# Optimization experiments

Measured on AMD Instinct MI355X. Metric: run time of the kernel, lower is better.

The kernel has to match this reference:

```python
import jax, jax.numpy as jnp
import numpy as np

ROPE_BASE = 10000.0


def _rope_cos_sin(seq_len, head_size, dtype):
    inv_freq = 1.0 / (ROPE_BASE ** (jnp.arange(0, head_size, 2, dtype=jnp.float32) / head_size))
    t = jnp.arange(seq_len, dtype=jnp.float32)
    freqs = jnp.outer(t, inv_freq)            # [S, D/2]
    emb = jnp.concatenate([freqs, freqs], axis=-1)  # [S, D]
    return jnp.cos(emb).astype(dtype), jnp.sin(emb).astype(dtype)


def _rotate_half(x):
    d = x.shape[-1] // 2
    return jnp.concatenate([-x[..., d:], x[..., :d]], axis=-1)


def setup_inputs() -> dict:
    key = jax.random.key(0)
    k1, k2, k3 = jax.random.split(key, 3)
    B, S, H, D = 2, 2048, 32, 128
    NUM_BLOCKS, BLOCK_SIZE = 512, 16
    q = jax.random.normal(k1, (B, S, H, D), dtype=jnp.float32)
    k = jax.random.normal(k2, (B, S, H, D), dtype=jnp.float32)
    v = jax.random.normal(k3, (B, S, H, D), dtype=jnp.float32)
    k_cache = jnp.zeros((NUM_BLOCKS, H, D, BLOCK_SIZE), dtype=jnp.float32)
    v_cache = jnp.zeros((NUM_BLOCKS, H, D, BLOCK_SIZE), dtype=jnp.float32)
    context_lengths = jnp.full((B,), S, dtype=jnp.int64)
    block_tables = jnp.arange(B * (S // BLOCK_SIZE), dtype=jnp.int64).reshape(B, S // BLOCK_SIZE)
    return {"q": q, "k": k, "v": v, "k_cache": k_cache, "v_cache": v_cache,
            "context_lengths": context_lengths, "block_tables": block_tables}


def reference(q, k, v, k_cache, v_cache, context_lengths, block_tables):
    # PagedAttention.pad_context_forward (prefill path, lengths == seq_len, block-aligned)
    B, S, H, D = q.shape
    block_size = k_cache.shape[-1]
    n_blk = S // block_size

    qt = q.transpose(0, 2, 1, 3)  # [B,H,S,D]
    kt = k.transpose(0, 2, 1, 3)
    vt = v.transpose(0, 2, 1, 3)

    cos, sin = _rope_cos_sin(S, D, q.dtype)  # [S,D], broadcast over B,H
    q_rot = qt * cos + _rotate_half(qt) * sin
    k_rot = kt * cos + _rotate_half(kt) * sin

    # copy_to_cache (prefill): scatter rotated keys and raw values into paged caches
    def to_blocks(x_bshd):  # [B,S,H,D] -> [B*n_blk, H, D, block_size]
        xb = x_bshd.reshape(B, n_blk, block_size, H, D)
        return xb.transpose(0, 1, 3, 4, 2).reshape(B * n_blk, H, D, block_size)

    k_cache_new = k_cache.at[block_tables.reshape(-1)].set(to_blocks(k_rot.transpose(0, 2, 1, 3)))
    v_cache_new = v_cache.at[block_tables.reshape(-1)].set(to_blocks(v))

    # dense causal attention, fp32 softmax
    scores = jnp.einsum('bhqd,bhkd->bhqk', q_rot, k_rot) / jnp.sqrt(jnp.asarray(D, q.dtype))
    causal = jnp.tril(jnp.ones((S, S), dtype=bool))
    scores = scores + jnp.where(causal, jnp.asarray(0.0, q.dtype), jnp.finfo(q.dtype).min)
    weights = jax.nn.softmax(scores.astype(jnp.float32), axis=-1).astype(q.dtype)
    out = jnp.einsum('bhqk,bhkd->bhqd', weights, vt)  # note: original uses un-rotated v
    attn_output = out.transpose(0, 2, 1, 3).reshape(B, S, H * D)
    return attn_output, k_cache_new, v_cache_new
```

## Files before the change

kernel.cpp:

```cpp
#include <hip/hip_runtime.h>
#include <math.h>

#define B 2
#define S 2048
#define H 32
#define D 128
#define BS 16
#define NBLK (S / BS)
#define NT 256

#define FREQ_C 0.20762050593045953f
#define SCALE 0.08838834764831845f

typedef __attribute__((ext_vector_type(8))) short short8;
typedef __attribute__((ext_vector_type(4))) float floatx4;

__device__ __forceinline__ unsigned short f2bf(float x) {
  return (unsigned short)((__float_as_uint(x) + 0x8000u) >> 16);
}
__device__ __forceinline__ unsigned packbf(float lo, float hi) {
  unsigned ua = __float_as_uint(lo) + 0x8000u;
  unsigned ub = __float_as_uint(hi) + 0x8000u;
  return (ub & 0xFFFF0000u) | (ua >> 16);
}

__device__ __forceinline__ void gload_lds16(const void* g, void* l) {
  __builtin_amdgcn_global_load_lds(
      (const __attribute__((address_space(1))) void*)g,
      (__attribute__((address_space(3))) void*)l, 16, 0, 0);
}

__global__ __launch_bounds__(256) void build_tbl(float* __restrict__ tbl) {
  int i = blockIdx.x * 256 + threadIdx.x;
  int s = i >> 6, j = i & 63;
  float fr = exp2f(-(float)j * FREQ_C);
  float sn, cs;
  sincosf((float)s * fr, &sn, &cs);
  tbl[s * 128 + j] = cs;
  tbl[s * 128 + 64 + j] = sn;
}

__global__ __launch_bounds__(512) void map_blocks(
    const int* __restrict__ bt, int* __restrict__ bitmap) {
  int t = threadIdx.x;
  bitmap[t] = 0;
  __syncthreads();
  if (t < B * NBLK) bitmap[bt[t]] = 1;
}

__global__ __launch_bounds__(256) void zero_unmapped(
    const int* __restrict__ bitmap, float* __restrict__ k_out,
    float* __restrict__ v_out) {
  int p = blockIdx.x;
  if (bitmap[p]) return;
  size_t base = (size_t)p * (H * D * BS) + (size_t)blockIdx.y * 8192;
  float4 z = {0.f, 0.f, 0.f, 0.f};
  float4* kd = (float4*)(k_out + base);
  float4* vd = (float4*)(v_out + base);
#pragma unroll
  for (int i = 0; i < 8; ++i) {
    kd[i * 256 + threadIdx.x] = z;
    vd[i * 256 + threadIdx.x] = z;
  }
}

__global__ __launch_bounds__(NT) void rope_scatter2(
    const float* __restrict__ k, const float* __restrict__ v,
    const int* __restrict__ block_tables,
    float* __restrict__ k_out, float* __restrict__ v_out,
    unsigned short* __restrict__ kvb, const float* __restrict__ tbl) {
  int idx = blockIdx.x;
  int h = idx % H;
  int m = idx / H;
  int b = m / NBLK;
  int sblk = m % NBLK;
  int phys = block_tables[m];

  __shared__ float Ks[BS][D + 4];
  __shared__ float Vs[BS][D + 4];
  __shared__ float Kr[BS][D + 4];
  __shared__ float Tc[BS][D + 4];
  int tid = threadIdx.x;

  const size_t in_base = (((size_t)b * S + (size_t)sblk * BS) * H + h) * D;
  const float* trow = tbl + (size_t)sblk * BS * 128;
  for (int p = 0; p < (BS * D) / NT; ++p) {
    int f = p * NT + tid;
    int row = f >> 7, d = f & 127;
    size_t g = in_base + (size_t)row * (H * D) + d;
    Ks[row][d] = k[g];
    Vs[row][d] = v[g];
    Tc[row][d] = trow[row * 128 + d];
  }
  __syncthreads();

  size_t out_base = ((size_t)phys * H + h) * (D * BS);
  for (int p = 0; p < (BS * D) / NT; ++p) {
    int f = p * NT + tid;
    int d = f >> 4, t = f & 15;
    float cs = Tc[t][d & 63];
    float sn = Tc[t][64 + (d & 63)];
    float x = Ks[t][d];
    float xr = (d < 64) ? -Ks[t][d + 64] : Ks[t][d - 64];
    float r = x * cs + xr * sn;
    k_out[out_base + f] = r;
    v_out[out_base + f] = Vs[t][d];
    Kr[t][d] = r;
  }
  __syncthreads();

  const int kt = sblk >> 2, cb = sblk & 3;
  const size_t tb = ((size_t)(b * H + h) * (S / 64) + kt) * 16384;
  unsigned* kb32 = (unsigned*)(kvb + tb) + (size_t)cb * 16 * 64;
  for (int p = 0; p < (BS * D / 2) / NT; ++p) {
    int e = p * NT + tid;
    int t = e >> 6, dp = e & 63;
    float2 kr2 = *(const float2*)&Kr[t][2 * dp];
    kb32[t * 64 + (dp ^ ((t & 7) << 2))] = packbf(kr2.x, kr2.y);
  }
  unsigned* vb32 = (unsigned*)(kvb + tb + 8192);
  for (int p = 0; p < (BS * D / 2) / NT; ++p) {
    int e = p * NT + tid;
    int d = e >> 3, tp = e & 7;
    vb32[d * 32 + ((cb * 8 + tp) ^ ((d & 7) << 2))] =
        packbf(Vs[2 * tp][d], Vs[2 * tp + 1][d]);
  }
}

__global__ __launch_bounds__(512, 4) void attn_mfma4(
    const float* __restrict__ q, const unsigned short* __restrict__ kvb,
    const float* __restrict__ tbl, float* __restrict__ out) {
  __shared__ unsigned short KV[2][16384];
  __shared__ unsigned short Pb[8][16][64];

  const int wgid = blockIdx.x;
  const int slot = wgid >> 3;
  const int bh = (slot >> 4) * 8 + (wgid & 7);
  const int qt = 15 - (slot & 15);
  const int b = bh >> 5, h = bh & 31;
  const int tid = threadIdx.x;
  const int lane = tid & 63, w = tid >> 6;
  const int n = lane & 15, quad = lane >> 4;

  short8 qf[4];
  {
    const int sq = qt * 128 + w * 16 + n;
    const float* qr = q + (((size_t)b * S + sq) * H + h) * D;
    const float* tr = tbl + (size_t)sq * 128;
#pragma unroll
    for (int ks = 0; ks < 4; ++ks) {
      int d0 = ks * 32 + quad * 8;
      float x[8], p[8], cs[8], sn[8];
      *(float4*)&x[0] = *(const float4*)(qr + d0);
      *(float4*)&x[4] = *(const float4*)(qr + d0 + 4);
      *(float4*)&p[0] = *(const float4*)(qr + (d0 ^ 64));
      *(float4*)&p[4] = *(const float4*)(qr + (d0 ^ 64) + 4);
      int dm = d0 & 63;
      *(float4*)&cs[0] = *(const float4*)(tr + dm);
      *(float4*)&cs[4] = *(const float4*)(tr + dm + 4);
      *(float4*)&sn[0] = *(const float4*)(tr + 64 + dm);
      *(float4*)&sn[4] = *(const float4*)(tr + 64 + dm + 4);
      unsigned short tmp[8];
#pragma unroll
      for (int i = 0; i < 8; ++i) {
        float r = (d0 < 64) ? (x[i] * cs[i] - p[i] * sn[i])
                            : (x[i] * cs[i] + p[i] * sn[i]);
        tmp[i] = f2bf(r * SCALE);
      }
      qf[ks] = *(short8*)tmp;
    }
  }

  const floatx4 zero = {0.f, 0.f, 0.f, 0.f};
  floatx4 Ot[8];
#pragma unroll
  for (int dt = 0; dt < 8; ++dt) Ot[dt] = zero;
  float m_run[4], l_run[4];
#pragma unroll
  for (int r = 0; r < 4; ++r) {
    m_run[r] = -INFINITY;
    l_run[r] = 0.f;
  }

  const unsigned short* KVg = kvb + (size_t)bh * (S / 64) * 16384;

  auto STAGE = [&](int buf, int t2) {
    const char* src =
        (const char*)(KVg + (size_t)t2 * 16384) + w * 4096 + (lane << 4);
    char* dst = (char*)&KV[buf][0] + w * 4096;
#pragma unroll
    for (int i = 0; i < 4; ++i) gload_lds16(src + i * 1024, dst + i * 1024);
  };

  const int last = 2 * qt + 1;
  int cur = 0;
  STAGE(0, 0);
  __syncthreads();

  const int sw = (n & 7) << 4;

  for (int kt = 0; kt <= last; ++kt) {
    if (kt < last) STAGE(cur ^ 1, kt + 1);

    const bool active = (kt * 64 <= qt * 128 + w * 16 + 15);
    if (active) {
      const char* Kb = (const char*)&KV[cur][0];
      const char* Vb = Kb + 16384;

      floatx4 acc[4];
#pragma unroll
      for (int ct = 0; ct < 4; ++ct) {
        floatx4 a = zero;
#pragma unroll
        for (int ks = 0; ks < 4; ++ks) {
          short8 kf = *(const short8*)(
              Kb + (((ct * 16 + n) * 256 + ks * 64 + quad * 16) ^ sw));
          a = __builtin_amdgcn_mfma_f32_16x16x32_bf16(qf[ks], kf, a, 0, 0, 0);
        }
        acc[ct] = a;
      }

      if (kt >= 2 * qt) {
        int lim = w * 16 + quad * 4 - (kt - 2 * qt) * 64;
#pragma unroll
        for (int ct = 0; ct < 4; ++ct)
#pragma unroll
          for (int r = 0; r < 4; ++r)
            if (ct * 16 + n > lim + r) acc[ct][r] = -INFINITY;
      }

      float mnew[4], alpha[4], rs[4];
#pragma unroll
      for (int r = 0; r < 4; ++r) {
        float v =
            fmaxf(fmaxf(acc[0][r], acc[1][r]), fmaxf(acc[2][r], acc[3][r]));
        v = fmaxf(v, __shfl_xor(v, 1));
        v = fmaxf(v, __shfl_xor(v, 2));
        v = fmaxf(v, __shfl_xor(v, 4));
        v = fmaxf(v, __shfl_xor(v, 8));
        mnew[r] = fmaxf(m_run[r], v);
        alpha[r] = __expf(m_run[r] - mnew[r]);
        m_run[r] = mnew[r];
      }
      float pv[4][4];
#pragma unroll
      for (int r = 0; r < 4; ++r) rs[r] = 0.f;
#pragma unroll
      for (int ct = 0; ct < 4; ++ct)
#pragma unroll
        for (int r = 0; r < 4; ++r) {
          float e = __expf(acc[ct][r] - mnew[r]);
          pv[ct][r] = e;
          rs[r] += e;
        }
#pragma unroll
      for (int r = 0; r < 4; ++r) {
        float s = rs[r];
        s += __shfl_xor(s, 1);
        s += __shfl_xor(s, 2);
        s += __shfl_xor(s, 4);
        s += __shfl_xor(s, 8);
        l_run[r] = l_run[r] * alpha[r] + s;
      }

#pragma unroll
      for (int dt = 0; dt < 8; ++dt)
#pragma unroll
        for (int r = 0; r < 4; ++r) Ot[dt][r] *= alpha[r];

#pragma unroll
      for (int ct = 0; ct < 4; ++ct)
#pragma unroll
        for (int r = 0; r < 4; ++r) {
          int row = quad * 4 + r;
          Pb[w][row][(ct * 16 + n) ^ ((row & 7) << 3)] = f2bf(pv[ct][r]);
        }
      __builtin_amdgcn_wave_barrier();

      short8 pf0 = *(const short8*)&Pb[w][n][(quad * 8) ^ ((n & 7) << 3)];
      short8 pf1 = *(const short8*)&Pb[w][n][(32 + quad * 8) ^ ((n & 7) << 3)];
#pragma unroll
      for (int dt = 0; dt < 8; ++dt) {
        short8 vf0 = *(const short8*)(
            Vb + (((dt * 16 + n) * 128 + quad * 16) ^ sw));
        short8 vf1 = *(const short8*)(
            Vb + (((dt * 16 + n) * 128 + 64 + quad * 16) ^ sw));
        Ot[dt] =
            __builtin_amdgcn_mfma_f32_16x16x32_bf16(pf0, vf0, Ot[dt], 0, 0, 0);
        Ot[dt] =
            __builtin_amdgcn_mfma_f32_16x16x32_bf16(pf1, vf1, Ot[dt], 0, 0, 0);
      }
    }
    __syncthreads();
    cur ^= 1;
  }

  float linv[4];
#pragma unroll
  for (int r = 0; r < 4; ++r) linv[r] = 1.f / l_run[r];
#pragma unroll
  for (int r = 0; r < 4; ++r) {
    int row = qt * 128 + w * 16 + quad * 4 + r;
    float* orow = out + ((size_t)(b * S + row) * H + h) * D + n;
#pragma unroll
    for (int dt = 0; dt < 8; ++dt) orow[dt * 16] = Ot[dt][r] * linv[r];
  }
}

__global__ __launch_bounds__(NT) void rope_scatter(
    const float* __restrict__ k, const float* __restrict__ v,
    const int* __restrict__ block_tables,
    float* __restrict__ k_out, float* __restrict__ v_out) {
  int idx = blockIdx.x;
  int h = idx % H;
  int m = idx / H;
  int b = m / NBLK;
  int sblk = m % NBLK;
  int phys = block_tables[m];

  __shared__ float Ks[BS][D + 4];
  __shared__ float Vs[BS][D + 4];
  int tid = threadIdx.x;

  const size_t in_base = (((size_t)b * S + (size_t)sblk * BS) * H + h) * D;
  for (int p = 0; p < (BS * D) / NT; ++p) {
    int f = p * NT + tid;
    int row = f >> 7, d = f & 127;
    size_t g = in_base + (size_t)row * (H * D) + d;
    Ks[row][d] = k[g];
    Vs[row][d] = v[g];
  }
  __syncthreads();

  size_t out_base = ((size_t)phys * H + h) * (D * BS);
  for (int p = 0; p < (BS * D) / NT; ++p) {
    int f = p * NT + tid;
    int d = f >> 4, t = f & 15;
    int s = sblk * BS + t;
    float fr = exp2f(-(float)(d & 63) * FREQ_C);
    float sn, cs;
    sincosf((float)s * fr, &sn, &cs);
    float x = Ks[t][d];
    float xr = (d < 64) ? -Ks[t][d + 64] : Ks[t][d - 64];
    k_out[out_base + f] = x * cs + xr * sn;
    v_out[out_base + f] = Vs[t][d];
  }
}

__global__ __launch_bounds__(NT, 3) void attn_mfma(
    const float* __restrict__ q, const float* __restrict__ kc,
    const float* __restrict__ vc, const int* __restrict__ bt,
    float* __restrict__ out) {
  __shared__ unsigned short Ks[64][136];
  __shared__ unsigned short Vt[128][72];
  __shared__ unsigned short Pb[4][16][72];

  const int qt = (S / 64 - 1) - (int)blockIdx.x;
  const int bh = blockIdx.y;
  const int b = bh >> 5, h = bh & 31;
  const int tid = threadIdx.x;
  const int lane = tid & 63, w = tid >> 6;
  const int n = lane & 15, quad = lane >> 4;

  short8 qf[4];
  {
    const int sq = qt * 64 + w * 16 + n;
    const float* qr = q + (((size_t)b * S + sq) * H + h) * D;
#pragma unroll
    for (int ks = 0; ks < 4; ++ks) {
      int d0 = ks * 32 + quad * 8;
      float x[8], p[8];
      *(float4*)&x[0] = *(const float4*)(qr + d0);
      *(float4*)&x[4] = *(const float4*)(qr + d0 + 4);
      *(float4*)&p[0] = *(const float4*)(qr + (d0 ^ 64));
      *(float4*)&p[4] = *(const float4*)(qr + (d0 ^ 64) + 4);
      unsigned short tmp[8];
#pragma unroll
      for (int i = 0; i < 8; ++i) {
        int d = d0 + i;
        float fr = exp2f(-(float)(d & 63) * FREQ_C);
        float sn, cs;
        __sincosf((float)sq * fr, &sn, &cs);
        float r = (d < 64) ? (x[i] * cs - p[i] * sn) : (x[i] * cs + p[i] * sn);
        tmp[i] = f2bf(r * SCALE);
      }
      qf[ks] = *(short8*)tmp;
    }
  }

  const floatx4 zero = {0.f, 0.f, 0.f, 0.f};
  floatx4 Ot[8];
#pragma unroll
  for (int dt = 0; dt < 8; ++dt) Ot[dt] = zero;
  float m_run[4], l_run[4];
#pragma unroll
  for (int r = 0; r < 4; ++r) {
    m_run[r] = -INFINITY;
    l_run[r] = 0.f;
  }

  for (int kt = 0; kt <= qt; ++kt) {
    int m4 = b * NBLK + kt * 4;
#pragma unroll
    for (int cb = 0; cb < 4; ++cb) {
      const size_t cbase = ((size_t)bt[m4 + cb] * H + h) * (D * BS);
      const float* ks_src = kc + cbase;
      const float* vs_src = vc + cbase;
#pragma unroll
      for (int it = 0; it < 4; ++it) {
        int rem = it * NT + tid;
        int dp = rem >> 4, t = rem & 15;
        float a0 = ks_src[(2 * dp) * BS + t];
        float a1 = ks_src[(2 * dp + 1) * BS + t];
        *(unsigned*)&Ks[cb * 16 + t][2 * dp] = packbf(a0, a1);
      }
#pragma unroll
      for (int it = 0; it < 4; ++it) {
        int rem = it * NT + tid;
        int d = rem >> 3, tp = rem & 7;
        float2 vv = *(const float2*)(vs_src + d * BS + tp * 2);
        *(unsigned*)&Vt[d][cb * 16 + tp * 2] = packbf(vv.x, vv.y);
      }
    }
    __syncthreads();

    floatx4 acc[4];
#pragma unroll
    for (int ct = 0; ct < 4; ++ct) {
      floatx4 a = zero;
#pragma unroll
      for (int ks = 0; ks < 4; ++ks) {
        short8 kf = *(const short8*)&Ks[ct * 16 + n][ks * 32 + quad * 8];
        a = __builtin_amdgcn_mfma_f32_16x16x32_bf16(qf[ks], kf, a, 0, 0, 0);
      }
      acc[ct] = a;
    }

    if (kt == qt) {
#pragma unroll
      for (int ct = 0; ct < 4; ++ct)
#pragma unroll
        for (int r = 0; r < 4; ++r)
          if (ct * 16 + n > w * 16 + quad * 4 + r) acc[ct][r] = -INFINITY;
    }

    float mnew[4], alpha[4], rs[4];
#pragma unroll
    for (int r = 0; r < 4; ++r) {
      float v = fmaxf(fmaxf(acc[0][r], acc[1][r]), fmaxf(acc[2][r], acc[3][r]));
      v = fmaxf(v, __shfl_xor(v, 1));
      v = fmaxf(v, __shfl_xor(v, 2));
      v = fmaxf(v, __shfl_xor(v, 4));
      v = fmaxf(v, __shfl_xor(v, 8));
      mnew[r] = fmaxf(m_run[r], v);
      alpha[r] = __expf(m_run[r] - mnew[r]);
      m_run[r] = mnew[r];
    }
    float pv[4][4];
#pragma unroll
    for (int r = 0; r < 4; ++r) rs[r] = 0.f;
#pragma unroll
    for (int ct = 0; ct < 4; ++ct)
#pragma unroll
      for (int r = 0; r < 4; ++r) {
        float e = __expf(acc[ct][r] - mnew[r]);
        pv[ct][r] = e;
        rs[r] += e;
      }
#pragma unroll
    for (int r = 0; r < 4; ++r) {
      float s = rs[r];
      s += __shfl_xor(s, 1);
      s += __shfl_xor(s, 2);
      s += __shfl_xor(s, 4);
      s += __shfl_xor(s, 8);
      l_run[r] = l_run[r] * alpha[r] + s;
    }

#pragma unroll
    for (int dt = 0; dt < 8; ++dt)
#pragma unroll
      for (int r = 0; r < 4; ++r) Ot[dt][r] *= alpha[r];

#pragma unroll
    for (int ct = 0; ct < 4; ++ct)
#pragma unroll
      for (int r = 0; r < 4; ++r)
        Pb[w][quad * 4 + r][ct * 16 + n] = f2bf(pv[ct][r]);
    __builtin_amdgcn_wave_barrier();

    short8 pf0 = *(const short8*)&Pb[w][n][quad * 8];
    short8 pf1 = *(const short8*)&Pb[w][n][32 + quad * 8];
#pragma unroll
    for (int dt = 0; dt < 8; ++dt) {
      short8 vf0 = *(const short8*)&Vt[dt * 16 + n][quad * 8];
      short8 vf1 = *(const short8*)&Vt[dt * 16 + n][32 + quad * 8];
      Ot[dt] = __builtin_amdgcn_mfma_f32_16x16x32_bf16(pf0, vf0, Ot[dt], 0, 0, 0);
      Ot[dt] = __builtin_amdgcn_mfma_f32_16x16x32_bf16(pf1, vf1, Ot[dt], 0, 0, 0);
    }
    __syncthreads();
  }

  float linv[4];
#pragma unroll
  for (int r = 0; r < 4; ++r) linv[r] = 1.f / l_run[r];
#pragma unroll
  for (int r = 0; r < 4; ++r) {
    int row = qt * 64 + w * 16 + quad * 4 + r;
    float* orow = out + ((size_t)(b * S + row) * H + h) * D + n;
#pragma unroll
    for (int dt = 0; dt < 8; ++dt) orow[dt * 16] = Ot[dt][r] * linv[r];
  }
}

extern "C" void kernel_launch(void* const* d_in, const int* in_sizes, int n_in,
                              void* d_out, int out_size, void* d_ws,
                              size_t ws_size, hipStream_t stream) {
  const float* q = (const float*)d_in[0];
  const float* k = (const float*)d_in[1];
  const float* v = (const float*)d_in[2];
  const int* block_tables = (const int*)d_in[6];

  float* out_attn = (float*)d_out;
  float* out_kc = out_attn + (size_t)B * S * H * D;
  float* out_vc = out_kc + (size_t)512 * H * D * BS;

  const size_t kvb_shorts = (size_t)B * H * (S / 64) * 16384;
  const size_t tbl_floats = (size_t)S * 128;
  const size_t need = kvb_shorts * 2 + tbl_floats * 4 + 2048;

  if (d_ws != nullptr && ws_size >= need) {
    unsigned short* kvb = (unsigned short*)d_ws;
    float* tbl = (float*)(kvb + kvb_shorts);
    int* bitmap = (int*)(tbl + tbl_floats);

    map_blocks<<<1, 512, 0, stream>>>(block_tables, bitmap);
    zero_unmapped<<<dim3(512, 8), 256, 0, stream>>>(bitmap, out_kc, out_vc);

    build_tbl<<<(S * 64) / 256, 256, 0, stream>>>(tbl);
    rope_scatter2<<<B * NBLK * H, NT, 0, stream>>>(k, v, block_tables, out_kc,
                                                   out_vc, kvb, tbl);
    attn_mfma4<<<(S / 128) * B * H, 512, 0, stream>>>(q, kvb, tbl, out_attn);
  } else {
    hipMemsetAsync(out_kc, 0, (size_t)512 * H * D * BS * sizeof(float), stream);
    hipMemsetAsync(out_vc, 0, (size_t)512 * H * D * BS * sizeof(float), stream);
    rope_scatter<<<B * NBLK * H, NT, 0, stream>>>(k, v, block_tables, out_kc,
                                                  out_vc);
    dim3 grid(S / 64, B * H);
    attn_mfma<<<grid, NT, 0, stream>>>(q, out_kc, out_vc, block_tables,
                                       out_attn);
  }
}
```

Before: 854.3 us.

## Use lazy softmax rescaling, deferred row-sum reduction and MFMA priority hints

Flash-attention online softmax now rescales the running max and output accumulators only when some row's new max exceeds the stored max by more than a threshold of 8, checked with a wave vote. Per-lane partial row sums are kept and reduced across lanes once at the end instead of every tile. s_setprio is raised around the QK and PV MFMA loops to favour matrix issue. This removes per-tile shuffles and accumulator rescaling, but allows stale maxima, so exp values can reach up to e^8 before normalisation.

```diff
diff --git a/kernel.cpp b/kernel.cpp
--- a/kernel.cpp
+++ b/kernel.cpp
@@ -127,7 +127,7 @@
   }
 }
 
-__global__ __launch_bounds__(512, 4) void attn_mfma4(
+__global__ __launch_bounds__(512, 4) void attn_mfma5(
     const float* __restrict__ q, const unsigned short* __restrict__ kvb,
     const float* __restrict__ tbl, float* __restrict__ out) {
   __shared__ unsigned short KV[2][16384];
@@ -175,11 +175,11 @@
   floatx4 Ot[8];
 #pragma unroll
   for (int dt = 0; dt < 8; ++dt) Ot[dt] = zero;
-  float m_run[4], l_run[4];
+  float m_run[4], l_part[4];
 #pragma unroll
   for (int r = 0; r < 4; ++r) {
     m_run[r] = -INFINITY;
-    l_run[r] = 0.f;
+    l_part[r] = 0.f;
   }
 
   const unsigned short* KVg = kvb + (size_t)bh * (S / 64) * 16384;
@@ -208,6 +208,7 @@
       const char* Vb = Kb + 16384;
 
       floatx4 acc[4];
+      __builtin_amdgcn_s_setprio(1);
 #pragma unroll
       for (int ct = 0; ct < 4; ++ct) {
         floatx4 a = zero;
@@ -219,6 +220,7 @@
         }
         acc[ct] = a;
       }
+      __builtin_amdgcn_s_setprio(0);
 
       if (kt >= 2 * qt) {
         int lim = w * 16 + quad * 4 - (kt - 2 * qt) * 64;
@@ -229,44 +231,38 @@
             if (ct * 16 + n > lim + r) acc[ct][r] = -INFINITY;
       }
 
-      float mnew[4], alpha[4], rs[4];
-#pragma unroll
-      for (int r = 0; r < 4; ++r) {
-        float v =
+      float rmax[4];
+#pragma unroll
+      for (int r = 0; r < 4; ++r)
+        rmax[r] =
             fmaxf(fmaxf(acc[0][r], acc[1][r]), fmaxf(acc[2][r], acc[3][r]));
-        v = fmaxf(v, __shfl_xor(v, 1));
-        v = fmaxf(v, __shfl_xor(v, 2));
-        v = fmaxf(v, __shfl_xor(v, 4));
-        v = fmaxf(v, __shfl_xor(v, 8));
-        mnew[r] = fmaxf(m_run[r], v);
-        alpha[r] = __expf(m_run[r] - mnew[r]);
-        m_run[r] = mnew[r];
+      bool ok = true;
+#pragma unroll
+      for (int r = 0; r < 4; ++r) ok = ok && (rmax[r] - m_run[r] <= 8.f);
+      if (!__all(ok ? 1 : 0)) {
+#pragma unroll
+        for (int r = 0; r < 4; ++r) {
+          float v = rmax[r];
+          v = fmaxf(v, __shfl_xor(v, 1));
+          v = fmaxf(v, __shfl_xor(v, 2));
+          v = fmaxf(v, __shfl_xor(v, 4));
+          v = fmaxf(v, __shfl_xor(v, 8));
+          float mnew = fmaxf(m_run[r], v);
+          float alpha = __expf(m_run[r] - mnew);
+          m_run[r] = mnew;
+          l_part[r] *= alpha;
+#pragma unroll
+          for (int dt = 0; dt < 8; ++dt) Ot[dt][r] *= alpha;
+        }
       }
       float pv[4][4];
 #pragma unroll
-      for (int r = 0; r < 4; ++r) rs[r] = 0.f;
-#pragma unroll
       for (int ct = 0; ct < 4; ++ct)
 #pragma unroll
-        for (int r = 0; r < 4; ++r) {
-          float e = __expf(acc[ct][r] - mnew[r]);
-          pv[ct][r] = e;
-          rs[r] += e;
-        }
-#pragma unroll
-      for (int r = 0; r < 4; ++r) {
-        float s = rs[r];
-        s += __shfl_xor(s, 1);
-        s += __shfl_xor(s, 2);
-        s += __shfl_xor(s, 4);
-        s += __shfl_xor(s, 8);
-        l_run[r] = l_run[r] * alpha[r] + s;
-      }
-
-#pragma unroll
-      for (int dt = 0; dt < 8; ++dt)
-#pragma unroll
-        for (int r = 0; r < 4; ++r) Ot[dt][r] *= alpha[r];
+        for (int r = 0; r < 4; ++r) pv[ct][r] = __expf(acc[ct][r] - m_run[r]);
+#pragma unroll
+      for (int r = 0; r < 4; ++r)
+        l_part[r] += (pv[0][r] + pv[1][r]) + (pv[2][r] + pv[3][r]);
 
 #pragma unroll
       for (int ct = 0; ct < 4; ++ct)
@@ -279,6 +275,7 @@
 
       short8 pf0 = *(const short8*)&Pb[w][n][(quad * 8) ^ ((n & 7) << 3)];
       short8 pf1 = *(const short8*)&Pb[w][n][(32 + quad * 8) ^ ((n & 7) << 3)];
+      __builtin_amdgcn_s_setprio(1);
 #pragma unroll
       for (int dt = 0; dt < 8; ++dt) {
         short8 vf0 = *(const short8*)(
@@ -290,6 +287,7 @@
         Ot[dt] =
             __builtin_amdgcn_mfma_f32_16x16x32_bf16(pf1, vf1, Ot[dt], 0, 0, 0);
       }
+      __builtin_amdgcn_s_setprio(0);
     }
     __syncthreads();
     cur ^= 1;
@@ -297,7 +295,14 @@
 
   float linv[4];
 #pragma unroll
-  for (int r = 0; r < 4; ++r) linv[r] = 1.f / l_run[r];
+  for (int r = 0; r < 4; ++r) {
+    float s = l_part[r];
+    s += __shfl_xor(s, 1);
+    s += __shfl_xor(s, 2);
+    s += __shfl_xor(s, 4);
+    s += __shfl_xor(s, 8);
+    linv[r] = 1.f / s;
+  }
 #pragma unroll
   for (int r = 0; r < 4; ++r) {
     int row = qt * 128 + w * 16 + quad * 4 + r;
@@ -540,7 +545,7 @@
     build_tbl<<<(S * 64) / 256, 256, 0, stream>>>(tbl);
     rope_scatter2<<<B * NBLK * H, NT, 0, stream>>>(k, v, block_tables, out_kc,
                                                    out_vc, kvb, tbl);
-    attn_mfma4<<<(S / 128) * B * H, 512, 0, stream>>>(q, kvb, tbl, out_attn);
+    attn_mfma5<<<(S / 128) * B * H, 512, 0, stream>>>(q, kvb, tbl, out_attn);
   } else {
     hipMemsetAsync(out_kc, 0, (size_t)512 * H * D * BS * sizeof(float), stream);
     hipMemsetAsync(out_vc, 0, (size_t)512 * H * D * BS * sizeof(float), stream);
```

Result: faster. 755.7 us (-11.5%).
